# Kernel optimization log

Measured on AMD Instinct MI355X. Metric: run time of the kernel, lower is better.

The kernel has to match this reference:

```python
import jax, jax.numpy as jnp
import numpy as np

DIM = 256
H = 8
HD = DIM // H
FFN = 4 * DIM
SCALE = HD ** -0.5


def _layernorm(x, g, b):
    mu = jnp.mean(x, axis=-1, keepdims=True)
    var = jnp.var(x, axis=-1, keepdims=True)
    return (x - mu) * jax.lax.rsqrt(var + 1e-5) * g + b


def _mha(xq, xkv, p, prefix, bias=None):
    B, N, _ = xq.shape
    M = xkv.shape[1]
    q = (xq @ p[prefix + '_q_w'] + p[prefix + '_q_b']).reshape(B, N, H, HD).transpose(0, 2, 1, 3)
    k = (xkv @ p[prefix + '_k_w'] + p[prefix + '_k_b']).reshape(B, M, H, HD).transpose(0, 2, 1, 3)
    v = (xkv @ p[prefix + '_v_w'] + p[prefix + '_v_b']).reshape(B, M, H, HD).transpose(0, 2, 1, 3)
    attn = jnp.einsum('bhnd,bhmd->bhnm', q, k) * SCALE
    if bias is not None:
        attn = attn + bias
    attn = jax.nn.softmax(attn, axis=-1)
    out = jnp.einsum('bhnm,bhmd->bhnd', attn, v).transpose(0, 2, 1, 3).reshape(B, N, DIM)
    return out @ p[prefix + '_o_w'] + p[prefix + '_o_b']


def _ffn(x, p):
    h = jax.nn.gelu(x @ p['ffn_w1'] + p['ffn_b1'], approximate=False)
    return h @ p['ffn_w2'] + p['ffn_b2']


def setup_inputs() -> dict:
    key = jax.random.key(0)
    ks = iter(jax.random.split(key, 40))
    B, N = 4, 1024
    inp = {
        'src_feats': jax.random.normal(next(ks), (B, N, DIM), jnp.float32),
        'tgt_feats': jax.random.normal(next(ks), (B, N, DIM), jnp.float32),
        'src_geo_bias': jax.random.normal(next(ks), (B, H, N, N), jnp.float32),
        'tgt_geo_bias': jax.random.normal(next(ks), (B, H, N, N), jnp.float32),
    }
    s = 0.02
    for pre in ('sa', 'ca'):
        for nm in ('q', 'k', 'v', 'o'):
            inp[f'{pre}_{nm}_w'] = jax.random.normal(next(ks), (DIM, DIM), jnp.float32) * s
            inp[f'{pre}_{nm}_b'] = jnp.zeros((DIM,), jnp.float32)
    for nm in ('ln_sa', 'ln_ca', 'ln_ff'):
        inp[nm + '_g'] = jnp.ones((DIM,), jnp.float32)
        inp[nm + '_b'] = jnp.zeros((DIM,), jnp.float32)
    inp['ffn_w1'] = jax.random.normal(next(ks), (DIM, FFN), jnp.float32) * s
    inp['ffn_b1'] = jnp.zeros((FFN,), jnp.float32)
    inp['ffn_w2'] = jax.random.normal(next(ks), (FFN, DIM), jnp.float32) * s
    inp['ffn_b2'] = jnp.zeros((DIM,), jnp.float32)
    return inp


def reference(src_feats, tgt_feats, src_geo_bias, tgt_geo_bias,
              sa_q_w, sa_q_b, sa_k_w, sa_k_b, sa_v_w, sa_v_b, sa_o_w, sa_o_b,
              ca_q_w, ca_q_b, ca_k_w, ca_k_b, ca_v_w, ca_v_b, ca_o_w, ca_o_b,
              ln_sa_g, ln_sa_b, ln_ca_g, ln_ca_b, ln_ff_g, ln_ff_b,
              ffn_w1, ffn_b1, ffn_w2, ffn_b2):
    p = dict(sa_q_w=sa_q_w, sa_q_b=sa_q_b, sa_k_w=sa_k_w, sa_k_b=sa_k_b,
             sa_v_w=sa_v_w, sa_v_b=sa_v_b, sa_o_w=sa_o_w, sa_o_b=sa_o_b,
             ca_q_w=ca_q_w, ca_q_b=ca_q_b, ca_k_w=ca_k_w, ca_k_b=ca_k_b,
             ca_v_w=ca_v_w, ca_v_b=ca_v_b, ca_o_w=ca_o_w, ca_o_b=ca_o_b,
             ffn_w1=ffn_w1, ffn_b1=ffn_b1, ffn_w2=ffn_w2, ffn_b2=ffn_b2)
    # 1. geometric self-attention (pre-norm residual)
    src = src_feats + _mha(_layernorm(src_feats, ln_sa_g, ln_sa_b), _layernorm(src_feats, ln_sa_g, ln_sa_b), p, 'sa', src_geo_bias)
    tgt = tgt_feats + _mha(_layernorm(tgt_feats, ln_sa_g, ln_sa_b), _layernorm(tgt_feats, ln_sa_g, ln_sa_b), p, 'sa', tgt_geo_bias)
    # 2. cross-attention (both use post-self-attn normed feats)
    src_n = _layernorm(src, ln_ca_g, ln_ca_b)
    tgt_n = _layernorm(tgt, ln_ca_g, ln_ca_b)
    src = src + _mha(src_n, tgt_n, p, 'ca')
    tgt = tgt + _mha(tgt_n, src_n, p, 'ca')
    # 3. FFN
    src = src + _ffn(_layernorm(src, ln_ff_g, ln_ff_b), p)
    tgt = tgt + _ffn(_layernorm(tgt, ln_ff_g, ln_ff_b), p)
    return (src, tgt)
```

## Files before the change

### kernel.cpp

```cpp
#include <hip/hip_runtime.h>
#include <math.h>

#define DIM   256
#define NHEAD 8
#define HD    32
#define SEQ   1024
#define BATCH 4
#define ROWS  (BATCH * SEQ)
#define ROWS2 (2 * ROWS)
#define FFND  1024
#define QKVN  768
#define ATT_SCALE 0.17677669529663687f

typedef __attribute__((ext_vector_type(8))) short   bf16x8;
typedef __attribute__((ext_vector_type(4))) float   f32x4;

__device__ __forceinline__ unsigned short f2bf(float x) {
    unsigned u = __float_as_uint(x);
    unsigned r = (u + 0x7fffu + ((u >> 16) & 1u)) >> 16;
    return (unsigned short)r;
}

typedef const __attribute__((address_space(1))) unsigned int* glds_gp;
typedef __attribute__((address_space(3))) unsigned int*       glds_lp;
__device__ __forceinline__ void glds16(const void* g, void* l) {
    __builtin_amdgcn_global_load_lds((glds_gp)g, (glds_lp)l, 16, 0, 0);
}

__global__ __launch_bounds__(256) void ln_kernel(
        const float* __restrict__ x, const float* __restrict__ g,
        const float* __restrict__ b, unsigned short* __restrict__ y) {
    const int wid  = threadIdx.x >> 6;
    const int lane = threadIdx.x & 63;
    const int row  = blockIdx.x * 4 + wid;
    float4 xv = ((const float4*)(x + (size_t)row * DIM))[lane];
    float s = xv.x + xv.y + xv.z + xv.w;
    #pragma unroll
    for (int off = 32; off >= 1; off >>= 1) s += __shfl_xor(s, off, 64);
    const float mu = s * (1.0f / DIM);
    const float dx = xv.x - mu, dy = xv.y - mu, dz = xv.z - mu, dw = xv.w - mu;
    float sq = dx * dx + dy * dy + dz * dz + dw * dw;
    #pragma unroll
    for (int off = 32; off >= 1; off >>= 1) sq += __shfl_xor(sq, off, 64);
    const float rs = rsqrtf(sq * (1.0f / DIM) + 1e-5f);
    const float4 gv = ((const float4*)g)[lane];
    const float4 bv = ((const float4*)b)[lane];
    ushort4 o;
    o.x = f2bf(dx * rs * gv.x + bv.x);
    o.y = f2bf(dy * rs * gv.y + bv.y);
    o.z = f2bf(dz * rs * gv.z + bv.z);
    o.w = f2bf(dw * rs * gv.w + bv.w);
    ((ushort4*)(y + (size_t)row * DIM))[lane] = o;
}

__global__ __launch_bounds__(256) void ln2_kernel(
        const float* __restrict__ x0, const float* __restrict__ x1,
        const float* __restrict__ g, const float* __restrict__ b,
        unsigned short* __restrict__ y) {
    const int wid  = threadIdx.x >> 6;
    const int lane = threadIdx.x & 63;
    const int row  = blockIdx.x * 4 + wid;
    const float* x = (row < ROWS) ? (x0 + (size_t)row * DIM)
                                  : (x1 + (size_t)(row - ROWS) * DIM);
    float4 xv = ((const float4*)x)[lane];
    float s = xv.x + xv.y + xv.z + xv.w;
    #pragma unroll
    for (int off = 32; off >= 1; off >>= 1) s += __shfl_xor(s, off, 64);
    const float mu = s * (1.0f / DIM);
    const float dx = xv.x - mu, dy = xv.y - mu, dz = xv.z - mu, dw = xv.w - mu;
    float sq = dx * dx + dy * dy + dz * dz + dw * dw;
    #pragma unroll
    for (int off = 32; off >= 1; off >>= 1) sq += __shfl_xor(sq, off, 64);
    const float rs = rsqrtf(sq * (1.0f / DIM) + 1e-5f);
    const float4 gv = ((const float4*)g)[lane];
    const float4 bv = ((const float4*)b)[lane];
    ushort4 o;
    o.x = f2bf(dx * rs * gv.x + bv.x);
    o.y = f2bf(dy * rs * gv.y + bv.y);
    o.z = f2bf(dz * rs * gv.z + bv.z);
    o.w = f2bf(dw * rs * gv.w + bv.w);
    ((ushort4*)(y + (size_t)row * DIM))[lane] = o;
}

__global__ __launch_bounds__(256) void convert_weights(
        const float* __restrict__ sa_q_w, const float* __restrict__ sa_k_w,
        const float* __restrict__ sa_v_w, const float* __restrict__ ca_q_w,
        const float* __restrict__ ca_k_w, const float* __restrict__ ca_v_w,
        const float* __restrict__ sa_o_w, const float* __restrict__ ca_o_w,
        const float* __restrict__ ffn_w1, const float* __restrict__ ffn_w2,
        const float* __restrict__ sa_q_b, const float* __restrict__ sa_k_b,
        const float* __restrict__ sa_v_b, const float* __restrict__ ca_q_b,
        const float* __restrict__ ca_k_b, const float* __restrict__ ca_v_b,
        unsigned short* __restrict__ sa_qkv_wt, unsigned short* __restrict__ ca_qkv_wt,
        unsigned short* __restrict__ sa_o_wt,   unsigned short* __restrict__ ca_o_wt,
        unsigned short* __restrict__ ffn1_wt,   unsigned short* __restrict__ ffn2_wt,
        float* __restrict__ sa_qkv_bias, float* __restrict__ ca_qkv_bias) {
    int gid = blockIdx.x * 256 + threadIdx.x;
    if (gid < 196608) {
        int n = gid >> 8, k = gid & 255, nn = n & 255;
        const float* w = (n < 256) ? sa_q_w : (n < 512) ? sa_k_w : sa_v_w;
        sa_qkv_wt[gid] = f2bf(w[k * 256 + nn]);
        return;
    }
    gid -= 196608;
    if (gid < 196608) {
        int n = gid >> 8, k = gid & 255, nn = n & 255;
        const float* w = (n < 256) ? ca_q_w : (n < 512) ? ca_k_w : ca_v_w;
        ca_qkv_wt[gid] = f2bf(w[k * 256 + nn]);
        return;
    }
    gid -= 196608;
    if (gid < 65536) { int n = gid >> 8, k = gid & 255; sa_o_wt[gid] = f2bf(sa_o_w[k * 256 + n]); return; }
    gid -= 65536;
    if (gid < 65536) { int n = gid >> 8, k = gid & 255; ca_o_wt[gid] = f2bf(ca_o_w[k * 256 + n]); return; }
    gid -= 65536;
    if (gid < 262144) { int n = gid >> 8,  k = gid & 255;  ffn1_wt[gid] = f2bf(ffn_w1[k * 1024 + n]); return; }
    gid -= 262144;
    if (gid < 262144) { int n = gid >> 10, k = gid & 1023; ffn2_wt[gid] = f2bf(ffn_w2[k * 256 + n]);  return; }
    gid -= 262144;
    if (gid < 768) {
        sa_qkv_bias[gid] = (gid < 256) ? sa_q_b[gid] : (gid < 512) ? sa_k_b[gid - 256] : sa_v_b[gid - 512];
        return;
    }
    gid -= 768;
    if (gid < 768) {
        ca_qkv_bias[gid] = (gid < 256) ? ca_q_b[gid] : (gid < 512) ? ca_k_b[gid - 256] : ca_v_b[gid - 512];
    }
}

template <bool GELU, int MODE>
__global__ __launch_bounds__(256) void gemm_bf16(
        const unsigned short* __restrict__ A, const unsigned short* __restrict__ Wt,
        const float* __restrict__ bias,
        const float* __restrict__ res_lo, const float* __restrict__ res_hi,
        float* __restrict__ Cf, unsigned short* __restrict__ Cb,
        unsigned short* __restrict__ vt_g,
        int N, int K, int rsplit) {
    __shared__ unsigned short As[64 * 64];
    __shared__ unsigned short Ws[64 * 64];
    const int t = threadIdx.x;
    const int w = t >> 6, lane = t & 63, quad = lane >> 4, l16 = lane & 15;
    const int wm = w >> 1, wn = w & 1;
    const int m0 = blockIdx.y * 64, n0 = blockIdx.x * 64;
    const int srow = lane >> 3;
    const int schunk = (lane & 7) ^ srow;

    f32x4 acc[2][2];
    #pragma unroll
    for (int i = 0; i < 2; i++)
        #pragma unroll
        for (int j = 0; j < 2; j++)
            acc[i][j] = (f32x4){0.f, 0.f, 0.f, 0.f};

    for (int k0 = 0; k0 < K; k0 += 64) {
        #pragma unroll
        for (int q = 0; q < 2; q++) {
            const int r0 = w * 16 + q * 8;
            glds16(&A [(size_t)(m0 + r0 + srow) * K + k0 + schunk * 8], &As[r0 * 64]);
            glds16(&Wt[(size_t)(n0 + r0 + srow) * K + k0 + schunk * 8], &Ws[r0 * 64]);
        }
        __syncthreads();
        #pragma unroll
        for (int kc = 0; kc < 2; kc++) {
            bf16x8 af[2], bfr[2];
            #pragma unroll
            for (int i = 0; i < 2; i++) {
                const int ra = wm * 32 + i * 16 + l16;
                const int rb = wn * 32 + i * 16 + l16;
                af[i]  = *(const bf16x8*)&As[ra * 64 + (((kc * 4 + quad) ^ (l16 & 7)) * 8)];
                bfr[i] = *(const bf16x8*)&Ws[rb * 64 + (((kc * 4 + quad) ^ (l16 & 7)) * 8)];
            }
            #pragma unroll
            for (int i = 0; i < 2; i++)
                #pragma unroll
                for (int j = 0; j < 2; j++)
                    acc[i][j] = __builtin_amdgcn_mfma_f32_16x16x32_bf16(af[i], bfr[j], acc[i][j], 0, 0, 0);
        }
        __syncthreads();
    }

    const float* res = nullptr;
    if (MODE == 0 && res_lo)
        res = (m0 < rsplit) ? res_lo : (res_hi - (size_t)rsplit * N);

    #pragma unroll
    for (int i = 0; i < 2; i++) {
        #pragma unroll
        for (int j = 0; j < 2; j++) {
            const int n = n0 + wn * 32 + j * 16 + l16;
            const float bv = bias[n];
            #pragma unroll
            for (int r = 0; r < 4; r++) {
                const int m = m0 + wm * 32 + i * 16 + quad * 4 + r;
                float v = acc[i][j][r] + bv;
                if (GELU) v = 0.5f * v * (1.0f + erff(v * 0.70710678118654752f));
                if (MODE == 0) {
                    if (res) v += res[(size_t)m * N + n];
                    Cf[(size_t)m * N + n] = v;
                } else if (MODE == 1) {
                    Cb[(size_t)m * N + n] = f2bf(v);
                } else {
                    if (n0 < 512) {
                        Cb[(size_t)m * 512 + n] = f2bf(v);
                    } else {
                        const int nn = n - 512, h = nn >> 5, d = nn & 31;
                        const int side = m >> 12, bb = (m >> 10) & 3, seq = m & 1023;
                        vt_g[(size_t)(side * 32 + bb * 8 + h) * 32768 + d * 1024 + seq] = f2bf(v);
                    }
                }
            }
        }
    }
}

template <bool HAS_BIAS>
__global__ __launch_bounds__(256) void attn_mfma(
        const unsigned short* __restrict__ qk, const unsigned short* __restrict__ vt,
        const float* __restrict__ bias_src, const float* __restrict__ bias_tgt,
        unsigned short* __restrict__ AO, int cross) {
    extern __shared__ char smem[];
    unsigned short* Kss = (unsigned short*)smem;
    unsigned short* Vts = (unsigned short*)(smem + 4096);
    unsigned short* Pss = (unsigned short*)(smem + 8192);
    float*          Bls = (float*)(smem + 17408);

    const int t = threadIdx.x;
    const int w = t >> 6, lane = t & 63, quad = lane >> 4, l16 = lane & 15;
    const int bh = blockIdx.y;
    const int side = bh >> 5, b = (bh >> 3) & 3, h = bh & 7;
    const int q0 = blockIdx.x * 64;
    const int qbase  = side * ROWS + b * SEQ;
    const int kvside = cross ? (1 - side) : side;
    const int kvbase = kvside * ROWS + b * SEQ;
    const int bhv = kvside * 32 + b * 8 + h;

    const bf16x8 aq = *(const bf16x8*)&qk[(size_t)(qbase + q0 + w * 16 + l16) * 512 + h * HD + quad * 8];

    const float* brow = nullptr;
    if (HAS_BIAS)
        brow = (side ? bias_tgt : bias_src)
             + ((size_t)(b * NHEAD + h) * SEQ + q0 + w * 16) * SEQ;

    const int krow  = w * 16 + (lane >> 2);
    const int kslot = (lane & 3) ^ ((lane >> 2) & 3);
    const int vrow  = w * 8 + (lane >> 3);
    const int vslot = (lane & 7) ^ ((lane >> 3) & 7);
    const int b_r   = lane >> 4;
    const int b_c   = (lane & 15) * 4;

    float lsum[4] = {0.f, 0.f, 0.f, 0.f};
    f32x4 o0 = (f32x4){0.f, 0.f, 0.f, 0.f};
    f32x4 o1 = (f32x4){0.f, 0.f, 0.f, 0.f};

    if (HAS_BIAS) {
        #pragma unroll
        for (int q = 0; q < 4; q++)
            glds16(&brow[(size_t)(q * 4 + b_r) * SEQ + b_c],
                   &Bls[w * 1024 + q * 256]);
    }

    for (int kt = 0; kt < SEQ / 64; kt++) {
        __syncthreads();
        glds16(&qk[(size_t)(kvbase + kt * 64 + krow) * 512 + 256 + h * HD + kslot * 8],
               &Kss[w * 16 * 32]);
        glds16(&vt[(size_t)bhv * 32768 + (size_t)vrow * 1024 + kt * 64 + vslot * 8],
               &Vts[w * 8 * 64]);
        __syncthreads();
        if (HAS_BIAS && kt + 1 < SEQ / 64) {
            #pragma unroll
            for (int q = 0; q < 4; q++)
                glds16(&brow[(size_t)(q * 4 + b_r) * SEQ + (kt + 1) * 64 + b_c],
                       &Bls[((kt + 1) & 1) * 4096 + w * 1024 + q * 256]);
        }

        f32x4 s[4];
        #pragma unroll
        for (int st = 0; st < 4; st++) {
            const bf16x8 kf = *(const bf16x8*)&Kss[(st * 16 + l16) * 32 + ((quad ^ (l16 & 3)) * 8)];
            f32x4 z = (f32x4){0.f, 0.f, 0.f, 0.f};
            s[st] = __builtin_amdgcn_mfma_f32_16x16x32_bf16(aq, kf, z, 0, 0, 0);
        }

        const float* bb = HAS_BIAS ? &Bls[(kt & 1) * 4096 + w * 1024] : nullptr;
        #pragma unroll
        for (int st = 0; st < 4; st++) {
            #pragma unroll
            for (int r = 0; r < 4; r++) {
                float v = s[st][r] * ATT_SCALE;
                if (HAS_BIAS) v += bb[(quad * 4 + r) * 64 + st * 16 + l16];
                const float p = __expf(v);
                lsum[r] += p;
                Pss[(w * 16 + quad * 4 + r) * 72 + st * 16 + l16] = f2bf(p);
            }
        }

        #pragma unroll
        for (int c = 0; c < 2; c++) {
            const bf16x8 ap  = *(const bf16x8*)&Pss[(w * 16 + l16) * 72 + c * 32 + quad * 8];
            const int slot = (((c * 4 + quad) ^ (l16 & 7)) * 8);
            const bf16x8 bv0 = *(const bf16x8*)&Vts[l16 * 64 + slot];
            const bf16x8 bv1 = *(const bf16x8*)&Vts[(16 + l16) * 64 + slot];
            o0 = __builtin_amdgcn_mfma_f32_16x16x32_bf16(ap, bv0, o0, 0, 0, 0);
            o1 = __builtin_amdgcn_mfma_f32_16x16x32_bf16(ap, bv1, o1, 0, 0, 0);
        }
    }

    #pragma unroll
    for (int r = 0; r < 4; r++) {
        float l = lsum[r];
        #pragma unroll
        for (int off = 1; off < 16; off <<= 1) l += __shfl_xor(l, off, 64);
        const float inv = 1.0f / l;
        const size_t orow = (size_t)(qbase + q0 + w * 16 + quad * 4 + r) * DIM + h * HD;
        AO[orow + l16]      = f2bf(o0[r] * inv);
        AO[orow + 16 + l16] = f2bf(o1[r] * inv);
    }
}

extern "C" void kernel_launch(void* const* d_in, const int* in_sizes, int n_in,
                              void* d_out, int out_size, void* d_ws, size_t ws_size,
                              hipStream_t stream) {
    const float* src_feats    = (const float*)d_in[0];
    const float* tgt_feats    = (const float*)d_in[1];
    const float* src_geo_bias = (const float*)d_in[2];
    const float* tgt_geo_bias = (const float*)d_in[3];
    const float* sa_q_w = (const float*)d_in[4];
    const float* sa_q_b = (const float*)d_in[5];
    const float* sa_k_w = (const float*)d_in[6];
    const float* sa_k_b = (const float*)d_in[7];
    const float* sa_v_w = (const float*)d_in[8];
    const float* sa_v_b = (const float*)d_in[9];
    const float* sa_o_w = (const float*)d_in[10];
    const float* sa_o_b = (const float*)d_in[11];
    const float* ca_q_w = (const float*)d_in[12];
    const float* ca_q_b = (const float*)d_in[13];
    const float* ca_k_w = (const float*)d_in[14];
    const float* ca_k_b = (const float*)d_in[15];
    const float* ca_v_w = (const float*)d_in[16];
    const float* ca_v_b = (const float*)d_in[17];
    const float* ca_o_w = (const float*)d_in[18];
    const float* ca_o_b = (const float*)d_in[19];
    const float* ln_sa_g = (const float*)d_in[20];
    const float* ln_sa_b = (const float*)d_in[21];
    const float* ln_ca_g = (const float*)d_in[22];
    const float* ln_ca_b = (const float*)d_in[23];
    const float* ln_ff_g = (const float*)d_in[24];
    const float* ln_ff_b = (const float*)d_in[25];
    const float* ffn_w1  = (const float*)d_in[26];
    const float* ffn_b1  = (const float*)d_in[27];
    const float* ffn_w2  = (const float*)d_in[28];
    const float* ffn_b2  = (const float*)d_in[29];

    float* out = (float*)d_out;

    char* ws = (char*)d_ws;
    unsigned short* Xn = (unsigned short*)(ws);
    unsigned short* QK = (unsigned short*)(ws + (4  << 20));
    unsigned short* VT = (unsigned short*)(ws + (12 << 20));
    unsigned short* AO = (unsigned short*)(ws + (16 << 20));
    unsigned short* Hh = (unsigned short*)(ws + (4  << 20));
    char* wp = ws + (20 << 20);
    unsigned short* sa_qkv_wt = (unsigned short*)wp;  wp += 768 * 256 * 2;
    unsigned short* ca_qkv_wt = (unsigned short*)wp;  wp += 768 * 256 * 2;
    unsigned short* sa_o_wt   = (unsigned short*)wp;  wp += 256 * 256 * 2;
    unsigned short* ca_o_wt   = (unsigned short*)wp;  wp += 256 * 256 * 2;
    unsigned short* ffn1_wt   = (unsigned short*)wp;  wp += 1024 * 256 * 2;
    unsigned short* ffn2_wt   = (unsigned short*)wp;  wp += 256 * 1024 * 2;
    float* sa_qkv_bias = (float*)wp;  wp += 768 * 4;
    float* ca_qkv_bias = (float*)wp;  wp += 768 * 4;

    const dim3 blk(256);
    const dim3 attn_grid(SEQ / 64, 64);
    const int smem_sa = 17408 + 2 * 4096 * 4;
    const int smem_ca = 17408;

    convert_weights<<<dim3(4103), blk, 0, stream>>>(
        sa_q_w, sa_k_w, sa_v_w, ca_q_w, ca_k_w, ca_v_w, sa_o_w, ca_o_w,
        ffn_w1, ffn_w2, sa_q_b, sa_k_b, sa_v_b, ca_q_b, ca_k_b, ca_v_b,
        sa_qkv_wt, ca_qkv_wt, sa_o_wt, ca_o_wt, ffn1_wt, ffn2_wt,
        sa_qkv_bias, ca_qkv_bias);

    ln2_kernel<<<dim3(ROWS2 / 4), blk, 0, stream>>>(src_feats, tgt_feats, ln_sa_g, ln_sa_b, Xn);
    gemm_bf16<false, 2><<<dim3(QKVN / 64, ROWS2 / 64), blk, 0, stream>>>(
        Xn, sa_qkv_wt, sa_qkv_bias, nullptr, nullptr, nullptr, QK, VT, QKVN, DIM, ROWS);
    attn_mfma<true><<<attn_grid, blk, smem_sa, stream>>>(QK, VT, src_geo_bias, tgt_geo_bias, AO, 0);
    gemm_bf16<false, 0><<<dim3(DIM / 64, ROWS2 / 64), blk, 0, stream>>>(
        AO, sa_o_wt, sa_o_b, src_feats, tgt_feats, out, nullptr, nullptr, DIM, DIM, ROWS);

    ln_kernel<<<dim3(ROWS2 / 4), blk, 0, stream>>>(out, ln_ca_g, ln_ca_b, Xn);
    gemm_bf16<false, 2><<<dim3(QKVN / 64, ROWS2 / 64), blk, 0, stream>>>(
        Xn, ca_qkv_wt, ca_qkv_bias, nullptr, nullptr, nullptr, QK, VT, QKVN, DIM, ROWS);
    attn_mfma<false><<<attn_grid, blk, smem_ca, stream>>>(QK, VT, nullptr, nullptr, AO, 1);
    gemm_bf16<false, 0><<<dim3(DIM / 64, ROWS2 / 64), blk, 0, stream>>>(
        AO, ca_o_wt, ca_o_b, out, out + (size_t)ROWS * DIM, out, nullptr, nullptr, DIM, DIM, ROWS);

    ln_kernel<<<dim3(ROWS2 / 4), blk, 0, stream>>>(out, ln_ff_g, ln_ff_b, Xn);
    gemm_bf16<true, 1><<<dim3(FFND / 64, ROWS2 / 64), blk, 0, stream>>>(
        Xn, ffn1_wt, ffn_b1, nullptr, nullptr, nullptr, Hh, nullptr, FFND, DIM, ROWS);
    gemm_bf16<false, 0><<<dim3(DIM / 64, ROWS2 / 64), blk, 0, stream>>>(
        Hh, ffn2_wt, ffn_b2, out, out + (size_t)ROWS * DIM, out, nullptr, nullptr, DIM, FFND, ROWS);
}
```

Baseline: 488.5 us.

## Double-buffer attention K/V loads, stage GEMM epilogue in LDS, tile weight transpose

The attention kernel now double-buffers K/V (and bias) tiles using async global-to-LDS loads with explicit vmcnt waits and a single barrier per iteration, so the next tile's fetch overlaps the current tile's compute. The GEMM epilogue writes results to shared memory first and then emits coalesced vector stores, including the transposed V layout. Weight conversion switches from scattered per-element transposes to 64x64 shared-memory tiled transposes with vector stores. Together these target memory stalls and uncoalesced writes, at the cost of more LDS, hand-counted waitcnt logic that must match the issued loads exactly, and a changed K swizzle.

```diff
diff --git a/kernel.cpp b/kernel.cpp
--- a/kernel.cpp
+++ b/kernel.cpp
@@ -26,6 +26,8 @@
 __device__ __forceinline__ void glds16(const void* g, void* l) {
     __builtin_amdgcn_global_load_lds((glds_gp)g, (glds_lp)l, 16, 0, 0);
 }
+
+#define WAITVM(N) __builtin_amdgcn_s_waitcnt(0x0F70 | ((N) & 0xF) | (((N) >> 4) << 14))
 
 __global__ __launch_bounds__(256) void ln_kernel(
         const float* __restrict__ x, const float* __restrict__ g,
@@ -95,36 +97,54 @@
         unsigned short* __restrict__ sa_o_wt,   unsigned short* __restrict__ ca_o_wt,
         unsigned short* __restrict__ ffn1_wt,   unsigned short* __restrict__ ffn2_wt,
         float* __restrict__ sa_qkv_bias, float* __restrict__ ca_qkv_bias) {
-    int gid = blockIdx.x * 256 + threadIdx.x;
-    if (gid < 196608) {
-        int n = gid >> 8, k = gid & 255, nn = n & 255;
-        const float* w = (n < 256) ? sa_q_w : (n < 512) ? sa_k_w : sa_v_w;
-        sa_qkv_wt[gid] = f2bf(w[k * 256 + nn]);
+    const int bid = blockIdx.x, t = threadIdx.x;
+    if (bid >= 256) {
+        const float* qb = (bid == 256) ? sa_q_b : ca_q_b;
+        const float* kb = (bid == 256) ? sa_k_b : ca_k_b;
+        const float* vb = (bid == 256) ? sa_v_b : ca_v_b;
+        float* ob = (bid == 256) ? sa_qkv_bias : ca_qkv_bias;
+        for (int e = t; e < 768; e += 256)
+            ob[e] = (e < 256) ? qb[e] : (e < 512) ? kb[e - 256] : vb[e - 512];
         return;
     }
-    gid -= 196608;
-    if (gid < 196608) {
-        int n = gid >> 8, k = gid & 255, nn = n & 255;
-        const float* w = (n < 256) ? ca_q_w : (n < 512) ? ca_k_w : ca_v_w;
-        ca_qkv_wt[gid] = f2bf(w[k * 256 + nn]);
-        return;
-    }
-    gid -= 196608;
-    if (gid < 65536) { int n = gid >> 8, k = gid & 255; sa_o_wt[gid] = f2bf(sa_o_w[k * 256 + n]); return; }
-    gid -= 65536;
-    if (gid < 65536) { int n = gid >> 8, k = gid & 255; ca_o_wt[gid] = f2bf(ca_o_w[k * 256 + n]); return; }
-    gid -= 65536;
-    if (gid < 262144) { int n = gid >> 8,  k = gid & 255;  ffn1_wt[gid] = f2bf(ffn_w1[k * 1024 + n]); return; }
-    gid -= 262144;
-    if (gid < 262144) { int n = gid >> 10, k = gid & 1023; ffn2_wt[gid] = f2bf(ffn_w2[k * 256 + n]);  return; }
-    gid -= 262144;
-    if (gid < 768) {
-        sa_qkv_bias[gid] = (gid < 256) ? sa_q_b[gid] : (gid < 512) ? sa_k_b[gid - 256] : sa_v_b[gid - 512];
-        return;
-    }
-    gid -= 768;
-    if (gid < 768) {
-        ca_qkv_bias[gid] = (gid < 256) ? ca_q_b[gid] : (gid < 512) ? ca_k_b[gid - 256] : ca_v_b[gid - 512];
+    const float* src; unsigned short* dst;
+    int Ns, Kd, sk, sn, dn;
+    if (bid < 96) {
+        int q = bid; const bool sa = q < 48; if (!sa) q -= 48;
+        const int kt = q & 3, nt = q >> 2, sub = nt >> 2;
+        src = sa ? (sub == 0 ? sa_q_w : sub == 1 ? sa_k_w : sa_v_w)
+                 : (sub == 0 ? ca_q_w : sub == 1 ? ca_k_w : ca_v_w);
+        dst = sa ? sa_qkv_wt : ca_qkv_wt;
+        Ns = 256; Kd = 256; sk = kt * 64; sn = (nt & 3) * 64; dn = nt * 64;
+    } else if (bid < 128) {
+        int q = bid - 96; const bool sa = q < 16; if (!sa) q -= 16;
+        const int kt = q & 3, nt = q >> 2;
+        src = sa ? sa_o_w : ca_o_w; dst = sa ? sa_o_wt : ca_o_wt;
+        Ns = 256; Kd = 256; sk = kt * 64; sn = nt * 64; dn = nt * 64;
+    } else if (bid < 192) {
+        const int q = bid - 128, kt = q & 3, nt = q >> 2;
+        src = ffn_w1; dst = ffn1_wt; Ns = 1024; Kd = 256;
+        sk = kt * 64; sn = nt * 64; dn = nt * 64;
+    } else {
+        const int q = bid - 192, kt = q & 15, nt = q >> 4;
+        src = ffn_w2; dst = ffn2_wt; Ns = 256; Kd = 1024;
+        sk = kt * 64; sn = nt * 64; dn = nt * 64;
+    }
+    __shared__ float T[64][65];
+    #pragma unroll
+    for (int p = 0; p < 4; p++) {
+        const int r = p * 16 + (t >> 4), c = (t & 15) * 4;
+        float4 v = *(const float4*)&src[(size_t)(sk + r) * Ns + sn + c];
+        T[r][c] = v.x; T[r][c + 1] = v.y; T[r][c + 2] = v.z; T[r][c + 3] = v.w;
+    }
+    __syncthreads();
+    #pragma unroll
+    for (int p = 0; p < 2; p++) {
+        const int nr = p * 32 + (t >> 3), kc = (t & 7) * 8;
+        bf16x8 o;
+        #pragma unroll
+        for (int e = 0; e < 8; e++) o[e] = (short)f2bf(T[kc + e][nr]);
+        *(bf16x8*)&dst[(size_t)(dn + nr) * Kd + sk + kc] = o;
     }
 }
 
@@ -136,8 +156,9 @@
         float* __restrict__ Cf, unsigned short* __restrict__ Cb,
         unsigned short* __restrict__ vt_g,
         int N, int K, int rsplit) {
-    __shared__ unsigned short As[64 * 64];
-    __shared__ unsigned short Ws[64 * 64];
+    __shared__ char smem[17408];
+    unsigned short* As = (unsigned short*)smem;
+    unsigned short* Ws = (unsigned short*)(smem + 8192);
     const int t = threadIdx.x;
     const int w = t >> 6, lane = t & 63, quad = lane >> 4, l16 = lane & 15;
     const int wm = w >> 1, wn = w & 1;
@@ -179,36 +200,57 @@
         __syncthreads();
     }
 
-    const float* res = nullptr;
-    if (MODE == 0 && res_lo)
-        res = (m0 < rsplit) ? res_lo : (res_hi - (size_t)rsplit * N);
-
+    const bool vpart = (MODE == 2) && (n0 >= 512);
+    float* Ctf = (float*)smem;
+    unsigned short* Ctb = (unsigned short*)smem;
     #pragma unroll
     for (int i = 0; i < 2; i++) {
         #pragma unroll
         for (int j = 0; j < 2; j++) {
-            const int n = n0 + wn * 32 + j * 16 + l16;
-            const float bv = bias[n];
+            const int nloc = wn * 32 + j * 16 + l16;
+            const float bv = bias[n0 + nloc];
             #pragma unroll
             for (int r = 0; r < 4; r++) {
-                const int m = m0 + wm * 32 + i * 16 + quad * 4 + r;
+                const int mloc = wm * 32 + i * 16 + quad * 4 + r;
                 float v = acc[i][j][r] + bv;
                 if (GELU) v = 0.5f * v * (1.0f + erff(v * 0.70710678118654752f));
-                if (MODE == 0) {
-                    if (res) v += res[(size_t)m * N + n];
-                    Cf[(size_t)m * N + n] = v;
-                } else if (MODE == 1) {
-                    Cb[(size_t)m * N + n] = f2bf(v);
-                } else {
-                    if (n0 < 512) {
-                        Cb[(size_t)m * 512 + n] = f2bf(v);
-                    } else {
-                        const int nn = n - 512, h = nn >> 5, d = nn & 31;
-                        const int side = m >> 12, bb = (m >> 10) & 3, seq = m & 1023;
-                        vt_g[(size_t)(side * 32 + bb * 8 + h) * 32768 + d * 1024 + seq] = f2bf(v);
-                    }
-                }
+                if (MODE == 0)       Ctf[mloc * 68 + nloc] = v;
+                else if (!vpart)     Ctb[mloc * 72 + nloc] = f2bf(v);
+                else                 Ctb[nloc * 72 + mloc] = f2bf(v);
             }
+        }
+    }
+    __syncthreads();
+    if (MODE == 0) {
+        const float* res = res_lo ? ((m0 < rsplit) ? res_lo : (res_hi - (size_t)rsplit * N))
+                                  : nullptr;
+        #pragma unroll
+        for (int p = 0; p < 4; p++) {
+            const int row = p * 16 + (t >> 4), c4 = (t & 15) * 4;
+            float4 v = *(float4*)&Ctf[row * 68 + c4];
+            const size_t go = (size_t)(m0 + row) * N + n0 + c4;
+            if (res) {
+                float4 rr = *(const float4*)&res[go];
+                v.x += rr.x; v.y += rr.y; v.z += rr.z; v.w += rr.w;
+            }
+            *(float4*)&Cf[go] = v;
+        }
+    } else if (!vpart) {
+        const int ldo = (MODE == 2) ? 512 : N;
+        #pragma unroll
+        for (int p = 0; p < 2; p++) {
+            const int row = p * 32 + (t >> 3), ch = (t & 7) * 8;
+            *(bf16x8*)&Cb[(size_t)(m0 + row) * ldo + n0 + ch] = *(bf16x8*)&Ctb[row * 72 + ch];
+        }
+    } else {
+        const int side = m0 >> 12, bb = (m0 >> 10) & 3, seq0 = m0 & 1023;
+        const int h0 = (n0 - 512) >> 5;
+        #pragma unroll
+        for (int p = 0; p < 2; p++) {
+            const int nl = p * 32 + (t >> 3), ch = (t & 7) * 8;
+            const int h = h0 + (nl >> 5), d = nl & 31;
+            *(bf16x8*)&vt_g[(size_t)(side * 32 + bb * 8 + h) * 32768 + d * 1024 + seq0 + ch]
+                = *(bf16x8*)&Ctb[nl * 72 + ch];
         }
     }
 }
@@ -218,11 +260,10 @@
         const unsigned short* __restrict__ qk, const unsigned short* __restrict__ vt,
         const float* __restrict__ bias_src, const float* __restrict__ bias_tgt,
         unsigned short* __restrict__ AO, int cross) {
-    extern __shared__ char smem[];
-    unsigned short* Kss = (unsigned short*)smem;
-    unsigned short* Vts = (unsigned short*)(smem + 4096);
-    unsigned short* Pss = (unsigned short*)(smem + 8192);
-    float*          Bls = (float*)(smem + 17408);
+    __shared__ unsigned short Kss[2 * 64 * 32];
+    __shared__ unsigned short Vts[2 * 32 * 64];
+    __shared__ unsigned short Pss[64 * 72];
+    __shared__ float Bls[HAS_BIAS ? 2 * 4096 : 4];
 
     const int t = threadIdx.x;
     const int w = t >> 6, lane = t & 63, quad = lane >> 4, l16 = lane & 15;
@@ -241,53 +282,61 @@
         brow = (side ? bias_tgt : bias_src)
              + ((size_t)(b * NHEAD + h) * SEQ + q0 + w * 16) * SEQ;
 
-    const int krow  = w * 16 + (lane >> 2);
-    const int kslot = (lane & 3) ^ ((lane >> 2) & 3);
-    const int vrow  = w * 8 + (lane >> 3);
-    const int vslot = (lane & 7) ^ ((lane >> 3) & 7);
-    const int b_r   = lane >> 4;
-    const int b_c   = (lane & 15) * 4;
+    const int krow  = lane >> 2;
+    const int kslot = (lane & 3) ^ (krow & 3) ^ ((krow >> 2) & 3);
+    const int vrow  = lane >> 3;
+    const int vslot = (lane & 7) ^ (vrow & 7);
+    const int kswz  = (quad ^ (l16 & 3) ^ ((l16 >> 2) & 3)) * 8;
+    const int brw   = lane >> 4;
+    const int bcl   = (lane & 15) * 4;
+
+    auto stageKV = [&](int kt, int buf) {
+        glds16(&qk[(size_t)(kvbase + kt * 64 + w * 16 + krow) * 512 + 256 + h * HD + kslot * 8],
+               &Kss[buf * 2048 + (w * 16) * 32]);
+        glds16(&vt[(size_t)bhv * 32768 + (size_t)(w * 8 + vrow) * 1024 + kt * 64 + vslot * 8],
+               &Vts[buf * 2048 + (w * 8) * 64]);
+    };
+    auto stageBias = [&](int kt, int buf) {
+        #pragma unroll
+        for (int g = 0; g < 4; g++)
+            glds16(&brow[(size_t)(g * 4 + brw) * SEQ + kt * 64 + bcl],
+                   &Bls[buf * 4096 + w * 1024 + g * 256]);
+    };
 
     float lsum[4] = {0.f, 0.f, 0.f, 0.f};
     f32x4 o0 = (f32x4){0.f, 0.f, 0.f, 0.f};
     f32x4 o1 = (f32x4){0.f, 0.f, 0.f, 0.f};
 
-    if (HAS_BIAS) {
-        #pragma unroll
-        for (int q = 0; q < 4; q++)
-            glds16(&brow[(size_t)(q * 4 + b_r) * SEQ + b_c],
-                   &Bls[w * 1024 + q * 256]);
-    }
-
-    for (int kt = 0; kt < SEQ / 64; kt++) {
-        __syncthreads();
-        glds16(&qk[(size_t)(kvbase + kt * 64 + krow) * 512 + 256 + h * HD + kslot * 8],
-               &Kss[w * 16 * 32]);
-        glds16(&vt[(size_t)bhv * 32768 + (size_t)vrow * 1024 + kt * 64 + vslot * 8],
-               &Vts[w * 8 * 64]);
-        __syncthreads();
-        if (HAS_BIAS && kt + 1 < SEQ / 64) {
-            #pragma unroll
-            for (int q = 0; q < 4; q++)
-                glds16(&brow[(size_t)(q * 4 + b_r) * SEQ + (kt + 1) * 64 + b_c],
-                       &Bls[((kt + 1) & 1) * 4096 + w * 1024 + q * 256]);
+    stageKV(0, 0);
+    if (HAS_BIAS) stageBias(0, 0);
+    WAITVM(HAS_BIAS ? 4 : 0);
+    __builtin_amdgcn_s_barrier();
+
+    for (int kt = 0; kt < 16; kt++) {
+        const int cb = kt & 1;
+        if (kt < 15) {
+            stageKV(kt + 1, cb ^ 1);
+            if (HAS_BIAS) stageBias(kt + 1, cb ^ 1);
         }
 
         f32x4 s[4];
         #pragma unroll
         for (int st = 0; st < 4; st++) {
-            const bf16x8 kf = *(const bf16x8*)&Kss[(st * 16 + l16) * 32 + ((quad ^ (l16 & 3)) * 8)];
+            const bf16x8 kf = *(const bf16x8*)&Kss[cb * 2048 + (st * 16 + l16) * 32 + kswz];
             f32x4 z = (f32x4){0.f, 0.f, 0.f, 0.f};
             s[st] = __builtin_amdgcn_mfma_f32_16x16x32_bf16(aq, kf, z, 0, 0, 0);
         }
 
-        const float* bb = HAS_BIAS ? &Bls[(kt & 1) * 4096 + w * 1024] : nullptr;
+        if (HAS_BIAS) {
+            if (kt < 15) WAITVM(6); else WAITVM(0);
+        }
+        const float* bb = HAS_BIAS ? &Bls[cb * 4096 + w * 1024] : nullptr;
         #pragma unroll
         for (int st = 0; st < 4; st++) {
             #pragma unroll
             for (int r = 0; r < 4; r++) {
                 float v = s[st][r] * ATT_SCALE;
-                if (HAS_BIAS) v += bb[(quad * 4 + r) * 64 + st * 16 + l16];
+                if (HAS_BIAS) v += bb[quad * 256 + r * 64 + st * 16 + l16];
                 const float p = __expf(v);
                 lsum[r] += p;
                 Pss[(w * 16 + quad * 4 + r) * 72 + st * 16 + l16] = f2bf(p);
@@ -298,10 +347,15 @@
         for (int c = 0; c < 2; c++) {
             const bf16x8 ap  = *(const bf16x8*)&Pss[(w * 16 + l16) * 72 + c * 32 + quad * 8];
             const int slot = (((c * 4 + quad) ^ (l16 & 7)) * 8);
-            const bf16x8 bv0 = *(const bf16x8*)&Vts[l16 * 64 + slot];
-            const bf16x8 bv1 = *(const bf16x8*)&Vts[(16 + l16) * 64 + slot];
+            const bf16x8 bv0 = *(const bf16x8*)&Vts[cb * 2048 + l16 * 64 + slot];
+            const bf16x8 bv1 = *(const bf16x8*)&Vts[cb * 2048 + (16 + l16) * 64 + slot];
             o0 = __builtin_amdgcn_mfma_f32_16x16x32_bf16(ap, bv0, o0, 0, 0, 0);
             o1 = __builtin_amdgcn_mfma_f32_16x16x32_bf16(ap, bv1, o1, 0, 0, 0);
+        }
+
+        if (kt < 15) {
+            WAITVM(HAS_BIAS ? 4 : 0);
+            __builtin_amdgcn_s_barrier();
         }
     }
 
@@ -371,10 +425,8 @@
 
     const dim3 blk(256);
     const dim3 attn_grid(SEQ / 64, 64);
-    const int smem_sa = 17408 + 2 * 4096 * 4;
-    const int smem_ca = 17408;
-
-    convert_weights<<<dim3(4103), blk, 0, stream>>>(
+
+    convert_weights<<<dim3(258), blk, 0, stream>>>(
         sa_q_w, sa_k_w, sa_v_w, ca_q_w, ca_k_w, ca_v_w, sa_o_w, ca_o_w,
         ffn_w1, ffn_w2, sa_q_b, sa_k_b, sa_v_b, ca_q_b, ca_k_b, ca_v_b,
         sa_qkv_wt, ca_qkv_wt, sa_o_wt, ca_o_wt, ffn1_wt, ffn2_wt,
@@ -383,14 +435,14 @@
     ln2_kernel<<<dim3(ROWS2 / 4), blk, 0, stream>>>(src_feats, tgt_feats, ln_sa_g, ln_sa_b, Xn);
     gemm_bf16<false, 2><<<dim3(QKVN / 64, ROWS2 / 64), blk, 0, stream>>>(
         Xn, sa_qkv_wt, sa_qkv_bias, nullptr, nullptr, nullptr, QK, VT, QKVN, DIM, ROWS);
-    attn_mfma<true><<<attn_grid, blk, smem_sa, stream>>>(QK, VT, src_geo_bias, tgt_geo_bias, AO, 0);
+    attn_mfma<true><<<attn_grid, blk, 0, stream>>>(QK, VT, src_geo_bias, tgt_geo_bias, AO, 0);
     gemm_bf16<false, 0><<<dim3(DIM / 64, ROWS2 / 64), blk, 0, stream>>>(
         AO, sa_o_wt, sa_o_b, src_feats, tgt_feats, out, nullptr, nullptr, DIM, DIM, ROWS);
 
     ln_kernel<<<dim3(ROWS2 / 4), blk, 0, stream>>>(out, ln_ca_g, ln_ca_b, Xn);
     gemm_bf16<false, 2><<<dim3(QKVN / 64, ROWS2 / 64), blk, 0, stream>>>(
         Xn, ca_qkv_wt, ca_qkv_bias, nullptr, nullptr, nullptr, QK, VT, QKVN, DIM, ROWS);
-    attn_mfma<false><<<attn_grid, blk, smem_ca, stream>>>(QK, VT, nullptr, nullptr, AO, 1);
+    attn_mfma<false><<<attn_grid, blk, 0, stream>>>(QK, VT, nullptr, nullptr, AO, 1);
     gemm_bf16<false, 0><<<dim3(DIM / 64, ROWS2 / 64), blk, 0, stream>>>(
         AO, ca_o_wt, ca_o_b, out, out + (size_t)ROWS * DIM, out, nullptr, nullptr, DIM, DIM, ROWS);
 
```

New measurement: 462.5 us. 5.3% less time.
